# Kernel optimization log

Measured on AMD Instinct MI355X. Metric: run time of the kernel, lower is better.

Reference implementation:

```python
import jax, jax.numpy as jnp
import numpy as np

N, C, H, W = 16, 128, 64, 64
SHIFT = 1  # fixed value of the init-time random.randint(-2, 2)
DN = ('NCHW', 'OIHW', 'NCHW')


def setup_inputs() -> dict:
    key = jax.random.key(0)
    ks = jax.random.split(key, 6)
    x = jax.random.normal(ks[0], (N, C, H, W), jnp.float32)
    p2 = jax.random.normal(ks[1], (1, C, 1, 1, W), jnp.float32) * 0.1   # trunc_normal std=0.1
    p3 = jax.random.normal(ks[2], (1, C, 7, 1, 1), jnp.float32) * 0.1
    p4 = jax.random.normal(ks[3], (1, C, H, W), jnp.float32) * 0.1
    w6 = jax.random.normal(ks[4], (C, 1, 3, 1), jnp.float32) * 0.1      # depthwise (3,1), dil (3,1)
    w7 = jax.random.normal(ks[5], (C * 7, C, 1, 7), jnp.float32) * 0.05 # dense (1,7)
    return {'x': x, 'p2': p2, 'p3': p3, 'p4': p4, 'w6': w6, 'w7': w7}


def reference(x, p2, p3, p4, w6, w7):
    n, c, h, w = x.shape
    # F.unfold(x, (7,1), dilation=(2,1), padding=(6,0)) -> (n, c, 7, h, w)
    xp = jnp.pad(x, ((0, 0), (0, 0), (6, 6), (0, 0)))
    t1 = jnp.stack([xp[:, :, 2 * k:2 * k + h, :] for k in range(7)], axis=2)
    t3 = p3 * (p2 * t1)                                   # fused gating multiplies
    t5 = jnp.roll(p4 * x, SHIFT, axis=3)
    t6 = jax.lax.conv_general_dilated(t5, w6, (1, 1), ((3, 3), (0, 0)),
                                      rhs_dilation=(3, 1), dimension_numbers=DN,
                                      feature_group_count=c)             # (n,c,h,w)
    t7 = jax.lax.conv_general_dilated(x, w7, (1, 1), ((0, 0), (3, 3)),
                                      dimension_numbers=DN)              # (n,7c,h,w)
    s = h * w
    t8 = jnp.einsum('ncs,nks->nck', x.reshape(n, c, s),
                    t3.reshape(n, c * 7, s)) / float(np.sqrt(s))         # (n,c,7c)
    t9 = jnp.einsum('nck,nks->ncs', t8,
                    t7.reshape(n, c * 7, s)) / float(np.sqrt(c * 7))
    return t9.reshape(n, c, h, w) - t6
```

## Files before the change

kernel.cpp:

```cpp
#include <hip/hip_runtime.h>

#define NB 16
#define CD 128
#define HD 64
#define WD 64
#define SD 4096
#define K7 896
#define XROW 72
#define SD2 4864

typedef float  f32x4  __attribute__((ext_vector_type(4)));
typedef __bf16 bf16x8 __attribute__((ext_vector_type(8)));
typedef __bf16 bf16x4 __attribute__((ext_vector_type(4)));

typedef __attribute__((address_space(3))) void lds_void_t;
typedef const __attribute__((address_space(1))) void gbl_void_t;

__device__ __forceinline__ void gl16(const void* g, void* l) {
  __builtin_amdgcn_global_load_lds((gbl_void_t*)g, (lds_void_t*)l, 16, 0, 0);
}

template<int N>
__device__ __forceinline__ void vw() {
  __builtin_amdgcn_sched_barrier(0);
  asm volatile("s_waitcnt vmcnt(%0)" :: "i"(N) : "memory");
  __builtin_amdgcn_s_barrier();
  __builtin_amdgcn_sched_barrier(0);
}
__device__ __forceinline__ void barr() {
  __builtin_amdgcn_sched_barrier(0);
  __builtin_amdgcn_s_barrier();
  __builtin_amdgcn_sched_barrier(0);
}

template<int N>
__device__ __forceinline__ void wbar() {
  __builtin_amdgcn_sched_barrier(0);
  asm volatile("s_waitcnt vmcnt(%0)" :: "i"(N) : "memory");
  __builtin_amdgcn_s_barrier();
  __builtin_amdgcn_sched_barrier(0);
}

__global__ __launch_bounds__(256)
void cvt_ximg(const float* __restrict__ x, const float* __restrict__ p2,
              __bf16* __restrict__ ximg, __bf16* __restrict__ xp2) {
  const int idx = (blockIdx.x * 256 + threadIdx.x) * 8;
  const float4 a = *(const float4*)(x + idx);
  const float4 b = *(const float4*)(x + idx + 4);
  bf16x8 v;
  v[0] = (__bf16)a.x; v[1] = (__bf16)a.y; v[2] = (__bf16)a.z; v[3] = (__bf16)a.w;
  v[4] = (__bf16)b.x; v[5] = (__bf16)b.y; v[6] = (__bf16)b.z; v[7] = (__bf16)b.w;
  const int plane = idx >> 12;
  const int n = plane >> 7, c = plane & 127;
  const int s0 = idx & 4095;
  const int stepg = s0 >> 5, kg = (s0 >> 3) & 3;
  *(bf16x8*)(ximg + ((size_t)((n * 128 + stepg) * 4 + kg) * 128 + c) * 8) = v;
  if (xp2) {
    const int j = s0 & 63;
    const float4 pa = *(const float4*)(p2 + c * 64 + j);
    const float4 pb = *(const float4*)(p2 + c * 64 + j + 4);
    bf16x8 w;
    w[0] = (__bf16)(a.x * pa.x); w[1] = (__bf16)(a.y * pa.y);
    w[2] = (__bf16)(a.z * pa.z); w[3] = (__bf16)(a.w * pa.w);
    w[4] = (__bf16)(b.x * pb.x); w[5] = (__bf16)(b.y * pb.y);
    w[6] = (__bf16)(b.z * pb.z); w[7] = (__bf16)(b.w * pb.w);
    *(bf16x8*)(xp2 + (size_t)plane * SD2 + 384 + s0) = w;
  }
}

__global__ __launch_bounds__(256)
void pad0_kernel(__bf16* __restrict__ xp2) {
  const int u = (blockIdx.x * 256 + threadIdx.x) * 8;
  const int plane = u / 768;
  const int r = u - plane * 768;
  const int off = (r < 384) ? r : (r + 4096);
  bf16x8 z = {};
  *(bf16x8*)(xp2 + (size_t)plane * SD2 + off) = z;
}

__global__ __launch_bounds__(256)
void w7img_kernel(const float* __restrict__ w7, const float* __restrict__ p3,
                  __bf16* __restrict__ w7img) {
  __shared__ float tile[64][65];
  const int b2 = blockIdx.x * 64;
  const int bp = blockIdx.y * 64;
  const int t  = threadIdx.x;
  const int col = t & 63;
  const int r0  = t >> 6;
#pragma unroll
  for (int rr = 0; rr < 16; ++rr) {
    const int row = rr * 4 + r0;
    tile[col][row] = w7[(size_t)(bp + row) * K7 + b2 + col];
  }
  __syncthreads();
  const int kpr = bp + col;
  const float p3v = p3[kpr];
#pragma unroll
  for (int rr = 0; rr < 16; ++rr) {
    const int row = rr * 4 + r0;
    const int k2  = b2 + row;
    const int c2  = k2 / 7, q = k2 - c2 * 7;
    const int k2q = q * 128 + c2;
    const size_t off = ((size_t)((k2q >> 6) * 28 + (kpr >> 5)) * 4 + ((kpr >> 3) & 3)) * 512
                     + (k2q & 63) * 8 + (kpr & 7);
    w7img[off] = (__bf16)(tile[row][col] * p3v);
  }
}

__global__ __launch_bounds__(256)
void xt_kernel(const float* __restrict__ x, __bf16* __restrict__ xT) {
  __shared__ __bf16 tile[128][72];
  const int n = blockIdx.y;
  const int i = blockIdx.x;
  const int t = threadIdx.x;
  const float* src = x + (size_t)n * CD * SD + (size_t)i * WD;
#pragma unroll
  for (int it = 0; it < 4; ++it) {
    const int c = it * 32 + (t >> 3);
    const int j = (t & 7) * 8;
    const float* s2 = src + (size_t)c * SD + j;
    const float4 a = *(const float4*)s2;
    const float4 b = *(const float4*)(s2 + 4);
    bf16x8 v;
    v[0] = (__bf16)a.x; v[1] = (__bf16)a.y; v[2] = (__bf16)a.z; v[3] = (__bf16)a.w;
    v[4] = (__bf16)b.x; v[5] = (__bf16)b.y; v[6] = (__bf16)b.z; v[7] = (__bf16)b.w;
    *(bf16x8*)&tile[c][j] = v;
  }
  __bf16* dstn = xT + ((size_t)n * HD + i) * XROW * CD;
  if (t < 128) {
    const int pr = t >> 4;
    const int rowz = pr < 3 ? pr : 64 + pr;
    bf16x8 z = {};
    *(bf16x8*)(dstn + (size_t)rowz * CD + (t & 15) * 8) = z;
  }
  __syncthreads();
#pragma unroll
  for (int it = 0; it < 4; ++it) {
    const int j   = t >> 2;
    const int c2b = (t & 3) * 32 + it * 8;
    bf16x8 v;
#pragma unroll
    for (int e = 0; e < 8; ++e) v[e] = tile[c2b + e][j];
    *(bf16x8*)(dstn + (size_t)(j + 3) * CD + c2b) = v;
  }
}

__global__ __launch_bounds__(256)
void p4t_kernel(const float* __restrict__ p4, __bf16* __restrict__ p4T) {
  __shared__ __bf16 tile[128][72];
  const int i = blockIdx.x;
  const int t = threadIdx.x;
#pragma unroll
  for (int it = 0; it < 4; ++it) {
    const int c = it * 32 + (t >> 3);
    const int j = (t & 7) * 8;
    const float* src = p4 + (size_t)c * SD + (size_t)i * WD + j;
    const float4 a = *(const float4*)src;
    const float4 b = *(const float4*)(src + 4);
    bf16x8 v;
    v[0] = (__bf16)a.x; v[1] = (__bf16)a.y; v[2] = (__bf16)a.z; v[3] = (__bf16)a.w;
    v[4] = (__bf16)b.x; v[5] = (__bf16)b.y; v[6] = (__bf16)b.z; v[7] = (__bf16)b.w;
    *(bf16x8*)&tile[c][j] = v;
  }
  __bf16* dst = p4T + (size_t)i * XROW * CD;
  if (t < 128) {
    const int pr = t >> 4;
    const int rowz = pr < 3 ? pr : 64 + pr;
    bf16x8 z = {};
    *(bf16x8*)(dst + (size_t)rowz * CD + (t & 15) * 8) = z;
  }
  __syncthreads();
#pragma unroll
  for (int it = 0; it < 4; ++it) {
    const int j   = t >> 2;
    const int c2b = (t & 3) * 32 + it * 8;
    bf16x8 v;
#pragma unroll
    for (int e = 0; e < 8; ++e) v[e] = tile[c2b + e][j];
    *(bf16x8*)(dst + (size_t)(j + 3) * CD + c2b) = v;
  }
}

template<int KC>
__global__ __launch_bounds__(256)
void reduce_img(const __bf16* __restrict__ part, __bf16* __restrict__ img,
                float scale) {
  const int idx8 = blockIdx.x * 256 + threadIdx.x;
  const int r = idx8 / 112;
  const int kchunk = idx8 - r * 112;
  const size_t in = (size_t)r * K7 + kchunk * 8;
  const size_t stride = (size_t)NB * CD * K7;
  float s[8];
  bf16x8 v = *(const bf16x8*)(part + in);
#pragma unroll
  for (int e = 0; e < 8; ++e) s[e] = (float)v[e];
#pragma unroll
  for (int c = 1; c < KC; ++c) {
    bf16x8 p = *(const bf16x8*)(part + c * stride + in);
#pragma unroll
    for (int e = 0; e < 8; ++e) s[e] += (float)p[e];
  }
  bf16x8 o;
#pragma unroll
  for (int e = 0; e < 8; ++e) o[e] = (__bf16)(s[e] * scale);
  const size_t out = ((size_t)(((r >> 7) * 28 + (kchunk >> 2)) * 4 + (kchunk & 3)) * 128
                      + (r & 127)) * 8;
  *(bf16x8*)(img + out) = o;
}

#define COMPUTE_STD(AB, BB)                                                     \
  do {                                                                          \
    bf16x8 af[4], bfr[2];                                                       \
    _Pragma("unroll")                                                           \
    for (int fm = 0; fm < 4; ++fm)                                              \
      af[fm] = *(const bf16x8*)&As[AB][(lg * 128 + wm * 64 + fm * 16 + l16) * 8]; \
    _Pragma("unroll")                                                           \
    for (int fn = 0; fn < 2; ++fn)                                              \
      bfr[fn] = *(const bf16x8*)&Bs[BB][(lg * 64 + wn * 32 + fn * 16 + l16) * 8]; \
    _Pragma("unroll")                                                           \
    for (int fm = 0; fm < 4; ++fm)                                              \
      _Pragma("unroll")                                                         \
      for (int fn = 0; fn < 2; ++fn)                                            \
        acc[fm][fn] = __builtin_amdgcn_mfma_f32_16x16x32_bf16(af[fm], bfr[fn],  \
                                                              acc[fm][fn], 0, 0, 0); \
  } while (0)

#define COMPUTE_SWZ(AB, BB, H)                                                  \
  do {                                                                          \
    bf16x8 af[4], bfr[2];                                                       \
    const int swz = ((((H) * 4 + lg) ^ (l16 & 7)) * 8);                         \
    _Pragma("unroll")                                                           \
    for (int fm = 0; fm < 4; ++fm)                                              \
      af[fm] = *(const bf16x8*)&As[AB][(lg * 128 + wm * 64 + fm * 16 + l16) * 8]; \
    _Pragma("unroll")                                                           \
    for (int fn = 0; fn < 2; ++fn)                                              \
      bfr[fn] = *(const bf16x8*)&Bs[BB][(wn * 32 + fn * 16 + l16) * 64 + swz];  \
    _Pragma("unroll")                                                           \
    for (int fm = 0; fm < 4; ++fm)                                              \
      _Pragma("unroll")                                                         \
      for (int fn = 0; fn < 2; ++fn)                                            \
        acc[fm][fn] = __builtin_amdgcn_mfma_f32_16x16x32_bf16(af[fm], bfr[fn],  \
                                                              acc[fm][fn], 0, 0, 0); \
  } while (0)

template<bool XP2>
__global__ __launch_bounds__(256)
void t8_mfma(const float* __restrict__ x, const __bf16* __restrict__ ximg,
             const __bf16* __restrict__ xp2, const float* __restrict__ p2,
             __bf16* __restrict__ part) {
  __shared__ __bf16 As[2][4096];
  __shared__ __bf16 Bs[2][4096];
  const int b = blockIdx.x;
  const int xcd = b & 7, slot0 = b >> 3;
  const int n  = xcd * 2 + slot0 / 56;
  const int r56 = slot0 % 56;
  const int kc = r56 / 14;
  const int n0 = (r56 % 14) * 64;
  const int t = threadIdx.x;
  const int lane = t & 63, wid = t >> 6;
  const int wm = wid & 1, wn = wid >> 1;
  const int l16 = lane & 15, lg = lane >> 4;
  const int wb = wid * 512;

  const __bf16* aptr = ximg + ((size_t)(n * 128 + kc * 32) * 512 + t) * 8;

  f32x4 acc[4][2] = {};

  if constexpr (XP2) {
    const int rl = lane >> 3;
    const int sl = lane & 7;
    const int ch = sl ^ rl;
    const int rA = wid * 16 + rl, rB = rA + 8;
    const int kpA = n0 + rA, kpB = n0 + rB;
    const int c2A = kpA / 7, kkA = kpA - c2A * 7;
    const int c2B = kpB / 7, kkB = kpB - c2B * 7;
    const __bf16* bptrA = xp2 + (size_t)(n * CD + c2A) * SD2
                        + (kc * 16 + 2 * kkA) * 64 + ch * 8;
    const __bf16* bptrB = xp2 + (size_t)(n * CD + c2B) * SD2
                        + (kc * 16 + 2 * kkB) * 64 + ch * 8;

#define T8A(B, ST) do {                                            \
    gl16(aptr + (size_t)(ST) * 4096,        &As[B][wb]);           \
    gl16(aptr + (size_t)(ST) * 4096 + 2048, &As[B][wb + 2048]);    \
  } while (0)
#define T8B(B, PP) do {                                            \
    gl16(bptrA + (PP) * 64, &Bs[B][wid * 1024]);                   \
    gl16(bptrB + (PP) * 64, &Bs[B][wid * 1024 + 512]);             \
  } while (0)

    const int P = 16;
    T8A(0, 0); T8B(0, 0);
    for (int p = 0; p < P - 1; ++p) {
      const int pb = p & 1;
      T8A(1, 2 * p + 1);
      T8B(pb ^ 1, p + 1);
      vw<4>();
      COMPUTE_SWZ(0, pb, 0);
      vw<2>();
      T8A(0, 2 * p + 2);
      COMPUTE_SWZ(1, pb, 1);
      barr();
    }
    { const int pb = (P - 1) & 1;
      T8A(1, 2 * P - 1);
      vw<2>();
      COMPUTE_SWZ(0, pb, 0);
      vw<0>();
      COMPUTE_SWZ(1, pb, 1);
    }
#undef T8A
#undef T8B
  } else {
    const int rw1 = wid * 16 + (lane >> 3);
    const int rw2 = rw1 + 8;
    const int kp1 = n0 + rw1, kp2 = n0 + rw2;
    const int c21 = kp1 / 7, kk1 = kp1 - c21 * 7;
    const int c22 = kp2 / 7, kk2 = kp2 - c22 * 7;
    const int scd = (lane & 7) ^ ((lane >> 3) & 7);
    const float* xr1 = x + ((size_t)n * CD + c21) * SD + scd * 8;
    const float* xr2 = x + ((size_t)n * CD + c22) * SD + scd * 8;
    float g1[8], g2[8];
#pragma unroll
    for (int e = 0; e < 8; ++e) {
      g1[e] = p2[c21 * WD + scd * 8 + e];
      g2[e] = p2[c22 * WD + scd * 8 + e];
    }
    const int d1 = rw1 * 64 + (lane & 7) * 8;
    const int d2 = d1 + 512;
    const int P = 16;
    float4 u10, u11, u20, u21;
    bool v1, v2;
#define T8A(B, ST) do {                                            \
    gl16(aptr + (size_t)(ST) * 4096,        &As[B][wb]);           \
    gl16(aptr + (size_t)(ST) * 4096 + 2048, &As[B][wb + 2048]);    \
  } while (0)
#define T8B_LOAD(PP) do {                                          \
    const int i_ = kc * 16 + (PP);                                 \
    const int ip1 = i_ + 2 * kk1 - 6, ip2 = i_ + 2 * kk2 - 6;      \
    v1 = ((unsigned)ip1 < (unsigned)HD);                           \
    v2 = ((unsigned)ip2 < (unsigned)HD);                           \
    if (v1) { u10 = *(const float4*)(xr1 + ip1 * 64);              \
              u11 = *(const float4*)(xr1 + ip1 * 64 + 4); }        \
    if (v2) { u20 = *(const float4*)(xr2 + ip2 * 64);              \
              u21 = *(const float4*)(xr2 + ip2 * 64 + 4); }        \
  } while (0)
#define T8B_WRITE(B) do {                                          \
    bf16x8 b1 = {}, b2 = {};                                       \
    if (v1) {                                                      \
      b1[0]=(__bf16)(u10.x*g1[0]); b1[1]=(__bf16)(u10.y*g1[1]);    \
      b1[2]=(__bf16)(u10.z*g1[2]); b1[3]=(__bf16)(u10.w*g1[3]);    \
      b1[4]=(__bf16)(u11.x*g1[4]); b1[5]=(__bf16)(u11.y*g1[5]);    \
      b1[6]=(__bf16)(u11.z*g1[6]); b1[7]=(__bf16)(u11.w*g1[7]);    \
    }                                                              \
    if (v2) {                                                      \
      b2[0]=(__bf16)(u20.x*g2[0]); b2[1]=(__bf16)(u20.y*g2[1]);    \
      b2[2]=(__bf16)(u20.z*g2[2]); b2[3]=(__bf16)(u20.w*g2[3]);    \
      b2[4]=(__bf16)(u21.x*g2[4]); b2[5]=(__bf16)(u21.y*g2[5]);    \
      b2[6]=(__bf16)(u21.z*g2[6]); b2[7]=(__bf16)(u21.w*g2[7]);    \
    }                                                              \
    *(bf16x8*)&Bs[B][d1] = b1;                                     \
    *(bf16x8*)&Bs[B][d2] = b2;                                     \
  } while (0)
    T8B_LOAD(0);
    T8A(0, 0);
    T8B_WRITE(0);
    __syncthreads();
    for (int p = 0; p < P; ++p) {
      const int pb = p & 1;
      if (p + 1 < P) T8B_LOAD(p + 1);
      T8A(1, 2 * p + 1);
      COMPUTE_SWZ(0, pb, 0);
      if (p + 1 < P) T8B_WRITE(pb ^ 1);
      __syncthreads();
      if (p + 1 < P) T8A(0, 2 * p + 2);
      COMPUTE_SWZ(1, pb, 1);
      __syncthreads();
    }
#undef T8A
#undef T8B_LOAD
#undef T8B_WRITE
  }

  const int colb = n0 + wn * 32 + l16;
  __bf16* pb2 = part + ((size_t)(kc * NB + n) * CD) * K7;
#pragma unroll
  for (int fm = 0; fm < 4; ++fm)
#pragma unroll
    for (int r2 = 0; r2 < 4; ++r2) {
      const int c1 = wm * 64 + fm * 16 + lg * 4 + r2;
      __bf16* orow = pb2 + (size_t)c1 * K7 + colb;
      orow[0]  = (__bf16)acc[fm][0][r2];
      orow[16] = (__bf16)acc[fm][1][r2];
    }
}

__global__ __launch_bounds__(256)
void m_mfma(const __bf16* __restrict__ t8img, const __bf16* __restrict__ w7img,
            __bf16* __restrict__ part) {
  __shared__ __bf16 As[4][4096];
  __shared__ __bf16 Bs[4][2048];
  const int tile = blockIdx.x;
  const int n    = blockIdx.y;
  const int kc   = blockIdx.z;
  const int t = threadIdx.x;
  const int lane = t & 63, wid = t >> 6;
  const int wm = wid & 1, wn = wid >> 1;
  const int l16 = lane & 15, lg = lane >> 4;
  const int wb = wid * 512;

  const __bf16* aptr = t8img + ((size_t)(n * 28 + kc * 14) * 512 + t) * 8;
  const __bf16* bptr = w7img + ((size_t)(tile * 28 + kc * 14) * 256 + t) * 8;

  f32x4 acc[4][2] = {};
  const int NSTEP = 14;

#define M_STG(B, ST) do {                                          \
    gl16(aptr + (size_t)(ST) * 4096,        &As[B][wb]);           \
    gl16(aptr + (size_t)(ST) * 4096 + 2048, &As[B][wb + 2048]);    \
    gl16(bptr + (size_t)(ST) * 2048,        &Bs[B][wb]);           \
  } while (0)

  M_STG(0, 0); M_STG(1, 1); M_STG(2, 2);
  for (int st = 0; st < NSTEP - 2; ++st) {
    wbar<6>();
    if (st + 3 < NSTEP) M_STG((st + 3) & 3, st + 3);
    COMPUTE_STD(st & 3, st & 3);
  }
  wbar<3>(); COMPUTE_STD((NSTEP - 2) & 3, (NSTEP - 2) & 3);
  wbar<0>(); COMPUTE_STD((NSTEP - 1) & 3, (NSTEP - 1) & 3);
#undef M_STG

  const int colb = tile * 64 + wn * 32 + l16;
  __bf16* pb = part + (size_t)kc * (NB * CD * K7);
#pragma unroll
  for (int fm = 0; fm < 4; ++fm)
#pragma unroll
    for (int r = 0; r < 4; ++r) {
      const int mr = n * 128 + wm * 64 + fm * 16 + lg * 4 + r;
      __bf16* orow = pb + (size_t)mr * K7 + colb;
      orow[0]  = (__bf16)acc[fm][0][r];
      orow[16] = (__bf16)acc[fm][1][r];
    }
}

__global__ __launch_bounds__(256)
void out_mfma(const __bf16* __restrict__ mimg, const __bf16* __restrict__ xT,
              const __bf16* __restrict__ p4T, const float* __restrict__ w6,
              float* __restrict__ outp) {
  __shared__ __bf16 As[2][4096];
  __shared__ __bf16 Bs[2][4096];
  const int b = blockIdx.x;
  const int xcd = b & 7, slot0 = b >> 3;
  const int n = (xcd << 1) | (slot0 >> 6);
  const int i = slot0 & 63;
  const int t = threadIdx.x;
  const int lane = t & 63, wid = t >> 6;
  const int wm = wid & 1, wn = wid >> 1;
  const int l16 = lane & 15, lg = lane >> 4;
  const int wb = wid * 512;

  const __bf16* aptr = mimg + ((size_t)n * 28 * 512 + t) * 8;

  const int colw = wid * 16 + (lane >> 3);
  const int scd8 = ((lane & 7) ^ ((lane >> 3) & 7)) * 8;
  const __bf16* bptr1 = xT + (((size_t)n * HD + i) * XROW + colw) * CD + scd8;
  const __bf16* bptr2 = bptr1 + 8 * CD;

  f32x4 acc[4][2] = {};

#define OA(B, ST) do {                                             \
    gl16(aptr + (size_t)(ST) * 4096,        &As[B][wb]);           \
    gl16(aptr + (size_t)(ST) * 4096 + 2048, &As[B][wb + 2048]);    \
  } while (0)
#define OB(B, PP) do {                                             \
    gl16(bptr1 + (PP) * 64, &Bs[B][wid * 1024]);                   \
    gl16(bptr2 + (PP) * 64, &Bs[B][wid * 1024 + 512]);             \
  } while (0)

  const int P = 14;
  OA(0, 0); OB(0, 0);
  for (int p = 0; p < P - 1; ++p) {
    const int pb = p & 1;
    OA(1, 2 * p + 1);
    OB(pb ^ 1, p + 1);
    vw<4>();
    COMPUTE_SWZ(0, pb, 0);
    vw<2>();
    OA(0, 2 * p + 2);
    COMPUTE_SWZ(1, pb, 1);
    barr();
  }
  { const int pb = (P - 1) & 1;
    OA(1, 2 * P - 1);
    vw<2>();
    COMPUTE_SWZ(0, pb, 0);
    vw<0>();
    COMPUTE_SWZ(1, pb, 1);
  }
#undef OA
#undef OB

  const __bf16* xTn = xT + (size_t)n * HD * XROW * CD;
#pragma unroll
  for (int fm = 0; fm < 4; ++fm) {
    const int cbase = wm * 64 + fm * 16 + lg * 4;
    const float4 wa  = *(const float4*)(w6 + cbase * 3);
    const float4 wbv = *(const float4*)(w6 + cbase * 3 + 4);
    const float4 wc  = *(const float4*)(w6 + cbase * 3 + 8);
    const float w6v[4][3] = {{wa.x, wa.y, wa.z}, {wa.w, wbv.x, wbv.y},
                             {wbv.z, wbv.w, wc.x}, {wc.y, wc.z, wc.w}};
#pragma unroll
    for (int fn = 0; fn < 2; ++fn) {
      const int jj = wn * 32 + fn * 16 + l16;
      const int jm = (jj - 1) & 63;
      const size_t ro = (size_t)(jm + 3) * CD + cbase;
      float t6v[4] = {0.f, 0.f, 0.f, 0.f};
#pragma unroll
      for (int rr = 0; rr < 3; ++rr) {
        const int ip = i + 3 * rr - 3;
        if ((unsigned)ip < (unsigned)HD) {
          const bf16x4 xv = *(const bf16x4*)(xTn + (size_t)ip * XROW * CD + ro);
          const bf16x4 pv = *(const bf16x4*)(p4T + (size_t)ip * XROW * CD + ro);
#pragma unroll
          for (int rq = 0; rq < 4; ++rq)
            t6v[rq] += w6v[rq][rr] * (float)pv[rq] * (float)xv[rq];
        }
      }
      float* obase = outp + ((size_t)(n * CD + cbase)) * SD + i * WD + jj;
#pragma unroll
      for (int rq = 0; rq < 4; ++rq)
        obase[(size_t)rq * SD] = acc[fm][fn][rq] - t6v[rq];
    }
  }
}

extern "C" void kernel_launch(void* const* d_in, const int* in_sizes, int n_in,
                              void* d_out, int out_size, void* d_ws, size_t ws_size,
                              hipStream_t stream) {
  const float* x  = (const float*)d_in[0];
  const float* p2 = (const float*)d_in[1];
  const float* p3 = (const float*)d_in[2];
  const float* p4 = (const float*)d_in[3];
  const float* w6 = (const float*)d_in[4];
  const float* w7 = (const float*)d_in[5];
  float* outp = (float*)d_out;

  const size_t e_x   = (size_t)NB * CD * SD;
  const size_t e_t8  = (size_t)NB * CD * K7;
  const size_t e_w7  = (size_t)K7 * K7;
  const size_t e_xp2 = (size_t)NB * CD * SD2;
  const size_t e_xT  = (size_t)NB * HD * XROW * CD;
  const size_t e_p4T = (size_t)HD * XROW * CD;

  const size_t base_b = (e_x + 2 * e_t8 + e_w7) * 2;
  const size_t xp2_b  = (e_xp2 + 4 * e_t8) * 2;
  const bool   tierA  = ws_size >= base_b + xp2_b;

  __bf16* ximg  = (__bf16*)d_ws;
  __bf16* t8img = ximg + e_x;
  __bf16* mimg  = t8img + e_t8;
  __bf16* w7img = mimg + e_t8;
  __bf16* region = w7img + e_w7;
  __bf16* xp2    = tierA ? region : nullptr;
  __bf16* partT8 = tierA ? (region + e_xp2) : region;
  __bf16* partM  = region;
  __bf16* xT     = region;
  __bf16* p4T    = region + e_xT;

  dim3 blk(256);
  cvt_ximg<<<dim3((unsigned)(e_x / 2048)), blk, 0, stream>>>(x, p2, ximg, xp2);
  if (tierA)
    pad0_kernel<<<dim3((unsigned)(NB * CD * 768 / 2048)), blk, 0, stream>>>(xp2);
  w7img_kernel<<<dim3(14, 14), blk, 0, stream>>>(w7, p3, w7img);

  if (tierA)
    t8_mfma<true><<<dim3(896), blk, 0, stream>>>(x, ximg, xp2, p2, partT8);
  else
    t8_mfma<false><<<dim3(896), blk, 0, stream>>>(x, ximg, nullptr, p2, partT8);
  reduce_img<4><<<dim3(896), blk, 0, stream>>>(partT8, t8img, 1.f / 64.f);

  m_mfma<<<dim3(14, 16, 2), blk, 0, stream>>>(t8img, w7img, partM);
  reduce_img<2><<<dim3(896), blk, 0, stream>>>(partM, mimg, 0.033407655f);

  xt_kernel<<<dim3(HD, NB), blk, 0, stream>>>(x, xT);
  p4t_kernel<<<dim3(HD), blk, 0, stream>>>(p4, p4T);
  out_mfma<<<dim3(1024), blk, 0, stream>>>(mimg, xT, p4T, w6, outp);
}
```

Baseline: 129.8 us.

## Deepen GEMM load pipeline to prefetch two stages ahead

In both MFMA GEMM kernels, the A-operand LDS buffer grows from two to four slots. Each stage's A and B tiles are now issued as a single group two stages ahead, right after the barrier. The compute loop waits once per stage, until only the next stage's loads are outstanding, instead of interleaving partial waits and loads between the two half-computes. This aims to hide more global-to-LDS latency, but raises LDS use per block from 32KB to 48KB, which may lower occupancy.

```diff
diff --git a/kernel.cpp b/kernel.cpp
--- a/kernel.cpp
+++ b/kernel.cpp
@@ -248,7 +248,7 @@
 void t8_mfma(const float* __restrict__ x, const __bf16* __restrict__ ximg,
              const __bf16* __restrict__ xp2, const float* __restrict__ p2,
              __bf16* __restrict__ part) {
-  __shared__ __bf16 As[2][4096];
+  __shared__ __bf16 As[XP2 ? 4 : 2][4096];
   __shared__ __bf16 Bs[2][4096];
   const int b = blockIdx.x;
   const int xcd = b & 7, slot0 = b >> 3;
@@ -279,37 +279,30 @@
     const __bf16* bptrB = xp2 + (size_t)(n * CD + c2B) * SD2
                         + (kc * 16 + 2 * kkB) * 64 + ch * 8;
 
-#define T8A(B, ST) do {                                            \
-    gl16(aptr + (size_t)(ST) * 4096,        &As[B][wb]);           \
-    gl16(aptr + (size_t)(ST) * 4096 + 2048, &As[B][wb + 2048]);    \
-  } while (0)
-#define T8B(B, PP) do {                                            \
-    gl16(bptrA + (PP) * 64, &Bs[B][wid * 1024]);                   \
-    gl16(bptrB + (PP) * 64, &Bs[B][wid * 1024 + 512]);             \
+#define TSTG(PP) do {                                                \
+    const int a0_ = (2 * (PP)) & 3, a1_ = (2 * (PP) + 1) & 3;        \
+    const int b_  = (PP) & 1;                                        \
+    gl16(aptr + (size_t)(2 * (PP)) * 4096,            &As[a0_][wb]); \
+    gl16(aptr + (size_t)(2 * (PP)) * 4096 + 2048,     &As[a0_][wb + 2048]); \
+    gl16(aptr + (size_t)(2 * (PP) + 1) * 4096,        &As[a1_][wb]); \
+    gl16(aptr + (size_t)(2 * (PP) + 1) * 4096 + 2048, &As[a1_][wb + 2048]); \
+    gl16(bptrA + (PP) * 64, &Bs[b_][wid * 1024]);                    \
+    gl16(bptrB + (PP) * 64, &Bs[b_][wid * 1024 + 512]);              \
   } while (0)
 
     const int P = 16;
-    T8A(0, 0); T8B(0, 0);
+    TSTG(0); TSTG(1);
     for (int p = 0; p < P - 1; ++p) {
-      const int pb = p & 1;
-      T8A(1, 2 * p + 1);
-      T8B(pb ^ 1, p + 1);
-      vw<4>();
-      COMPUTE_SWZ(0, pb, 0);
-      vw<2>();
-      T8A(0, 2 * p + 2);
-      COMPUTE_SWZ(1, pb, 1);
+      vw<6>();
+      COMPUTE_SWZ((2 * p) & 3, p & 1, 0);
+      COMPUTE_SWZ((2 * p + 1) & 3, p & 1, 1);
       barr();
+      if (p + 2 < P) TSTG(p + 2);
     }
-    { const int pb = (P - 1) & 1;
-      T8A(1, 2 * P - 1);
-      vw<2>();
-      COMPUTE_SWZ(0, pb, 0);
-      vw<0>();
-      COMPUTE_SWZ(1, pb, 1);
-    }
-#undef T8A
-#undef T8B
+    vw<0>();
+    COMPUTE_SWZ((2 * (P - 1)) & 3, (P - 1) & 1, 0);
+    COMPUTE_SWZ((2 * (P - 1) + 1) & 3, (P - 1) & 1, 1);
+#undef TSTG
   } else {
     const int rw1 = wid * 16 + (lane >> 3);
     const int rw2 = rw1 + 8;
@@ -447,7 +440,7 @@
 void out_mfma(const __bf16* __restrict__ mimg, const __bf16* __restrict__ xT,
               const __bf16* __restrict__ p4T, const float* __restrict__ w6,
               float* __restrict__ outp) {
-  __shared__ __bf16 As[2][4096];
+  __shared__ __bf16 As[4][4096];
   __shared__ __bf16 Bs[2][4096];
   const int b = blockIdx.x;
   const int xcd = b & 7, slot0 = b >> 3;
@@ -468,37 +461,30 @@
 
   f32x4 acc[4][2] = {};
 
-#define OA(B, ST) do {                                             \
-    gl16(aptr + (size_t)(ST) * 4096,        &As[B][wb]);           \
-    gl16(aptr + (size_t)(ST) * 4096 + 2048, &As[B][wb + 2048]);    \
-  } while (0)
-#define OB(B, PP) do {                                             \
-    gl16(bptr1 + (PP) * 64, &Bs[B][wid * 1024]);                   \
-    gl16(bptr2 + (PP) * 64, &Bs[B][wid * 1024 + 512]);             \
+#define OSTG(PP) do {                                                \
+    const int a0_ = (2 * (PP)) & 3, a1_ = (2 * (PP) + 1) & 3;        \
+    const int b_  = (PP) & 1;                                        \
+    gl16(aptr + (size_t)(2 * (PP)) * 4096,            &As[a0_][wb]); \
+    gl16(aptr + (size_t)(2 * (PP)) * 4096 + 2048,     &As[a0_][wb + 2048]); \
+    gl16(aptr + (size_t)(2 * (PP) + 1) * 4096,        &As[a1_][wb]); \
+    gl16(aptr + (size_t)(2 * (PP) + 1) * 4096 + 2048, &As[a1_][wb + 2048]); \
+    gl16(bptr1 + (PP) * 64, &Bs[b_][wid * 1024]);                    \
+    gl16(bptr2 + (PP) * 64, &Bs[b_][wid * 1024 + 512]);              \
   } while (0)
 
   const int P = 14;
-  OA(0, 0); OB(0, 0);
+  OSTG(0); OSTG(1);
   for (int p = 0; p < P - 1; ++p) {
-    const int pb = p & 1;
-    OA(1, 2 * p + 1);
-    OB(pb ^ 1, p + 1);
-    vw<4>();
-    COMPUTE_SWZ(0, pb, 0);
-    vw<2>();
-    OA(0, 2 * p + 2);
-    COMPUTE_SWZ(1, pb, 1);
+    vw<6>();
+    COMPUTE_SWZ((2 * p) & 3, p & 1, 0);
+    COMPUTE_SWZ((2 * p + 1) & 3, p & 1, 1);
     barr();
-  }
-  { const int pb = (P - 1) & 1;
-    OA(1, 2 * P - 1);
-    vw<2>();
-    COMPUTE_SWZ(0, pb, 0);
-    vw<0>();
-    COMPUTE_SWZ(1, pb, 1);
-  }
-#undef OA
-#undef OB
+    if (p + 2 < P) OSTG(p + 2);
+  }
+  vw<0>();
+  COMPUTE_SWZ((2 * (P - 1)) & 3, (P - 1) & 1, 0);
+  COMPUTE_SWZ((2 * (P - 1) + 1) & 3, (P - 1) & 1, 1);
+#undef OSTG
 
   const __bf16* xTn = xT + (size_t)n * HD * XROW * CD;
 #pragma unroll
```

After: 150.0 us, median of 5. +15.6%, slower.
